# Kernel tuning notes

Hardware: AMD Instinct MI355X
Metric: run time of the kernel (lower is better)

The kernel has to match this reference:

```python
import jax, jax.numpy as jnp
import numpy as np

NUM_DIHEDRALS = 3
# Idealized backbone geometry (picometers / radians), as in RGN/pNeRF.
BOND_LENGTHS = np.array([145.801, 152.326, 132.868], dtype=np.float32)  # N-CA, CA-C, C-N
BOND_ANGLES = np.array([2.124, 1.941, 2.028], dtype=np.float32)


def setup_inputs() -> dict:
    key = jax.random.key(0)
    num_steps, batch = 2048, 512
    flat_dihedrals = jax.random.uniform(
        key, (num_steps * batch, NUM_DIHEDRALS),
        minval=-np.pi, maxval=np.pi, dtype=jnp.float32)
    return {"flat_dihedrals": flat_dihedrals, "batch_size": batch}


def _l2_normalize(v, eps=1e-12):
    return v / jnp.sqrt(jnp.sum(v * v, axis=-1, keepdims=True) + eps)


def dihedral_to_point(dihedral):
    # dihedral: [L, B, 3] -> points in local frames: [3L, B, 3]
    r_cos_theta = np.float32(BOND_LENGTHS * np.cos(np.pi - BOND_ANGLES))  # [3]
    r_sin_theta = np.float32(BOND_LENGTHS * np.sin(np.pi - BOND_ANGLES))  # [3]
    L, B, _ = dihedral.shape
    pt_x = jnp.broadcast_to(jnp.asarray(r_cos_theta), (L, B, NUM_DIHEDRALS))
    pt_y = jnp.cos(dihedral) * r_sin_theta
    pt_z = jnp.sin(dihedral) * r_sin_theta
    point = jnp.stack([pt_x, pt_y, pt_z], axis=-1)      # [L, B, 3, 3]
    return point.reshape(L * NUM_DIHEDRALS, B, 3)       # [3L, B, 3]


def point_to_coordinate(points):
    # points: [N, B, 3]; sequential NeRF rigid-body chain extension.
    B = points.shape[1]
    init = np.array([[-np.sqrt(0.5), np.sqrt(1.5), 0.0],
                     [-np.sqrt(2.0), 0.0, 0.0],
                     [0.0, 0.0, 0.0]], dtype=np.float32)
    a = jnp.broadcast_to(jnp.asarray(init[0]), (B, 3))
    b = jnp.broadcast_to(jnp.asarray(init[1]), (B, 3))
    c = jnp.broadcast_to(jnp.asarray(init[2]), (B, 3))

    def step(carry, p):
        a, b, c = carry
        bc = _l2_normalize(c - b)                      # [B, 3]
        n = _l2_normalize(jnp.cross(b - a, bc))        # [B, 3]
        # Rotation matrix with columns [bc, n x bc, n]
        m = jnp.stack([bc, jnp.cross(n, bc), n], axis=-1)   # [B, 3, 3]
        coord = jnp.einsum('bij,bj->bi', m, p) + c          # [B, 3]
        return (b, c, coord), coord

    _, coords = jax.lax.scan(step, (a, b, c), points)
    return coords  # [N, B, 3]


def reference(flat_dihedrals, batch_size):
    num_steps = flat_dihedrals.shape[0] // batch_size
    dihedrals = flat_dihedrals.reshape(num_steps, batch_size, NUM_DIHEDRALS)
    points = dihedral_to_point(dihedrals)
    coordinates = point_to_coordinate(points)
    return coordinates
```

## Files before the change

kernel.cpp:

```cpp
#include <hip/hip_runtime.h>
#include <math.h>

#define BATCH 512
#define FRAGS 256
#define GROUP 16
#define NGRP  (FRAGS/GROUP)
#define BTILE 32
#define NTILE (BATCH/BTILE)
#define RPF   8
#define READY 0x5EADBEEF

__device__ __forceinline__ void compose(const float* A, const float* B, float* D) {
    float d[12];
    #pragma unroll
    for (int i = 0; i < 3; ++i) {
        #pragma unroll
        for (int j = 0; j < 3; ++j)
            d[i*3+j] = A[i*3+0]*B[0*3+j] + A[i*3+1]*B[1*3+j] + A[i*3+2]*B[2*3+j];
        d[9+i] = A[i*3+0]*B[9] + A[i*3+1]*B[10] + A[i*3+2]*B[11] + A[9+i];
    }
    #pragma unroll
    for (int k = 0; k < 12; ++k) D[k] = d[k];
}

__device__ __forceinline__ void set_identity(float* D) {
    D[0]=1.f; D[1]=0.f; D[2]=0.f;
    D[3]=0.f; D[4]=1.f; D[5]=0.f;
    D[6]=0.f; D[7]=0.f; D[8]=1.f;
    D[9]=0.f; D[10]=0.f; D[11]=0.f;
}

__device__ __forceinline__ void frame_of(
    float ax, float ay, float az,
    float bx, float by, float bz,
    float cx, float cy, float cz,
    float* out )
{
    float bcx = cx - bx, bcy = cy - by, bcz = cz - bz;
    float inv = rsqrtf(bcx*bcx + bcy*bcy + bcz*bcz + 1e-12f);
    bcx *= inv; bcy *= inv; bcz *= inv;
    float bax = bx - ax, bay = by - ay, baz = bz - az;
    float nx = bay*bcz - baz*bcy;
    float ny = baz*bcx - bax*bcz;
    float nz = bax*bcy - bay*bcx;
    inv = rsqrtf(nx*nx + ny*ny + nz*nz + 1e-12f);
    nx *= inv; ny *= inv; nz *= inv;
    float mx = ny*bcz - nz*bcy;
    float my = nz*bcx - nx*bcz;
    float mz = nx*bcy - ny*bcx;
    out[0] = bcx; out[1] = mx; out[2] = nx;
    out[3] = bcy; out[4] = my; out[5] = ny;
    out[6] = bcz; out[7] = mz; out[8] = nz;
    out[9] = cx; out[10] = cy; out[11] = cz;
}

__device__ __forceinline__ void nerf_step(
    float ax, float ay, float az,
    float bx, float by, float bz,
    float cx, float cy, float cz,
    float px, float py, float pz,
    float& ox, float& oy, float& oz)
{
    float bcx = cx - bx, bcy = cy - by, bcz = cz - bz;
    float inv = rsqrtf(bcx*bcx + bcy*bcy + bcz*bcz + 1e-12f);
    bcx *= inv; bcy *= inv; bcz *= inv;
    float bax = bx - ax, bay = by - ay, baz = bz - az;
    float nx = bay*bcz - baz*bcy;
    float ny = baz*bcx - bax*bcz;
    float nz = bax*bcy - bay*bcx;
    inv = rsqrtf(nx*nx + ny*ny + nz*nz + 1e-12f);
    nx *= inv; ny *= inv; nz *= inv;
    float mx = ny*bcz - nz*bcy;
    float my = nz*bcx - nx*bcz;
    float mz = nx*bcy - ny*bcx;
    ox = bcx*px + mx*py + nx*pz + cx;
    oy = bcy*px + my*py + ny*pz + cy;
    oz = bcz*px + mz*py + nz*pz + cz;
}

__device__ __forceinline__ void lane_consts(int b, float* rcl, float* rsl) {
    const float PI = 3.14159265358979323846f;
    float rc[3], rs[3];
    rc[0] = 145.801f * cosf(PI - 2.124f); rs[0] = 145.801f * sinf(PI - 2.124f);
    rc[1] = 152.326f * cosf(PI - 1.941f); rs[1] = 152.326f * sinf(PI - 1.941f);
    rc[2] = 132.868f * cosf(PI - 2.028f); rs[2] = 132.868f * sinf(PI - 2.028f);
    const int d0 = b % 3, d1 = (b + 2) % 3, d2 = (b + 1) % 3;
    rcl[0] = rc[d0]; rcl[1] = rc[d1]; rcl[2] = rc[d2];
    rsl[0] = rs[d0]; rsl[1] = rs[d1]; rsl[2] = rs[d2];
}

__global__ void __launch_bounds__(GROUP * BTILE) coord_onepass(
    const float* __restrict__ dih, float* __restrict__ T,
    int* __restrict__ flags, float* __restrict__ out)
{
    const int btile = blockIdx.x & (NTILE - 1);
    const int g     = blockIdx.x >> 4;
    const int bsub  = threadIdx.x & (BTILE - 1);
    const int j     = threadIdx.x >> 5;
    const int f     = g * GROUP + j;
    const int b     = btile * BTILE + bsub;

    __shared__ float BufA[GROUP * BTILE * 13];
    __shared__ float BufB[GROUP * BTILE * 13];
    float* rowA = &BufA[(size_t)threadIdx.x * 13];
    float* rowB = &BufB[(size_t)threadIdx.x * 13];

    float rcl[3], rsl[3];
    lane_consts(b, rcl, rsl);

    float dd[3 * RPF];
    #pragma unroll
    for (int r = 0; r < RPF; ++r) {
        const float* src = dih + (size_t)(f * RPF + r) * (3 * BATCH) + b;
        dd[r*3 + 0] = __builtin_nontemporal_load(src);
        dd[r*3 + 1] = __builtin_nontemporal_load(src + BATCH);
        dd[r*3 + 2] = __builtin_nontemporal_load(src + 2 * BATCH);
    }

    float lx[3 * RPF], ly[3 * RPF], lz[3 * RPF];

    float ax = -0.70710678118654752f, ay = 1.22474487139158905f, az = 0.0f;
    float bx = -1.41421356237309505f, by = 0.0f, bz = 0.0f;
    float cx = 0.0f, cy = 0.0f, cz = 0.0f;

    #pragma unroll
    for (int r = 0; r < RPF; ++r) {
        #pragma unroll
        for (int k = 0; k < 3; ++k) {
            float sn, cs;
            __sincosf(dd[r*3 + k], &sn, &cs);
            float ox, oy, oz;
            nerf_step(ax, ay, az, bx, by, bz, cx, cy, cz,
                      rcl[k], cs * rsl[k], sn * rsl[k], ox, oy, oz);
            ax = bx; ay = by; az = bz;
            bx = cx; by = cy; bz = cz;
            cx = ox; cy = oy; cz = oz;
            lx[r*3 + k] = ox; ly[r*3 + k] = oy; lz[r*3 + k] = oz;
        }
    }

    float cur[12];
    frame_of(ax, ay, az, bx, by, bz, cx, cy, cz, cur);

    #pragma unroll
    for (int k = 0; k < 12; ++k) rowA[k] = cur[k];
    __syncthreads();
    if (j >= 1) compose(&BufA[(size_t)(threadIdx.x - 1*BTILE) * 13], cur, cur);

    #pragma unroll
    for (int k = 0; k < 12; ++k) rowB[k] = cur[k];
    __syncthreads();
    if (j >= 2) compose(&BufB[(size_t)(threadIdx.x - 2*BTILE) * 13], cur, cur);

    #pragma unroll
    for (int k = 0; k < 12; ++k) rowA[k] = cur[k];
    __syncthreads();
    if (j >= 4) compose(&BufA[(size_t)(threadIdx.x - 4*BTILE) * 13], cur, cur);

    #pragma unroll
    for (int k = 0; k < 12; ++k) rowB[k] = cur[k];
    __syncthreads();
    if (j >= 8) compose(&BufB[(size_t)(threadIdx.x - 8*BTILE) * 13], cur, cur);

    #pragma unroll
    for (int k = 0; k < 12; ++k) rowA[k] = cur[k];
    __syncthreads();

    float pprev[12];
    if (j > 0) {
        #pragma unroll
        for (int k = 0; k < 12; ++k)
            pprev[k] = BufA[(size_t)(threadIdx.x - BTILE) * 13 + k];
    }

    if (j == GROUP - 1 && g < NGRP - 1) {
        #pragma unroll
        for (int k = 0; k < 12; ++k)
            __hip_atomic_store(&T[((size_t)g * 12 + k) * BATCH + b], cur[k],
                               __ATOMIC_RELAXED, __HIP_MEMORY_SCOPE_AGENT);
        if (bsub == 0)
            __hip_atomic_store(&flags[g * NTILE + btile], READY,
                               __ATOMIC_RELEASE, __HIP_MEMORY_SCOPE_AGENT);
    }

    float G[12];
    if (g == 0) {
        if (j == 0) set_identity(G);
        else {
            #pragma unroll
            for (int k = 0; k < 12; ++k) G[k] = pprev[k];
        }
    } else {
        float cur2[12];
        if (j < g) {
            while (__hip_atomic_load(&flags[j * NTILE + btile],
                                     __ATOMIC_ACQUIRE, __HIP_MEMORY_SCOPE_AGENT)
                   != READY) {
                __builtin_amdgcn_s_sleep(1);
            }
            #pragma unroll
            for (int k = 0; k < 12; ++k)
                cur2[k] = __hip_atomic_load(&T[((size_t)j * 12 + k) * BATCH + b],
                                            __ATOMIC_RELAXED, __HIP_MEMORY_SCOPE_AGENT);
        } else {
            set_identity(cur2);
        }

        #pragma unroll
        for (int k = 0; k < 12; ++k) rowB[k] = cur2[k];
        __syncthreads();
        if (j >= 1) compose(&BufB[(size_t)(threadIdx.x - 1*BTILE) * 13], cur2, cur2);

        #pragma unroll
        for (int k = 0; k < 12; ++k) rowA[k] = cur2[k];
        __syncthreads();
        if (j >= 2) compose(&BufA[(size_t)(threadIdx.x - 2*BTILE) * 13], cur2, cur2);

        #pragma unroll
        for (int k = 0; k < 12; ++k) rowB[k] = cur2[k];
        __syncthreads();
        if (j >= 4) compose(&BufB[(size_t)(threadIdx.x - 4*BTILE) * 13], cur2, cur2);

        #pragma unroll
        for (int k = 0; k < 12; ++k) rowA[k] = cur2[k];
        __syncthreads();
        if (j >= 8) compose(&BufA[(size_t)(threadIdx.x - 8*BTILE) * 13], cur2, cur2);

        #pragma unroll
        for (int k = 0; k < 12; ++k) rowB[k] = cur2[k];
        __syncthreads();
        float E[12];
        #pragma unroll
        for (int k = 0; k < 12; ++k)
            E[k] = BufB[(size_t)((g - 1) * BTILE + bsub) * 13 + k];

        if (j == 0) {
            #pragma unroll
            for (int k = 0; k < 12; ++k) G[k] = E[k];
        } else {
            compose(E, pprev, G);
        }
    }

    #pragma unroll
    for (int q = 0; q < 3 * RPF; ++q) {
        float ox = lx[q], oy = ly[q], oz = lz[q];
        float gx = G[0]*ox + G[1]*oy + G[2]*oz + G[9];
        float gy = G[3]*ox + G[4]*oy + G[5]*oz + G[10];
        float gz = G[6]*ox + G[7]*oy + G[8]*oz + G[11];
        size_t n = (size_t)f * (3 * RPF) + q;
        float* dst = out + (n * BATCH + b) * 3;
        __builtin_nontemporal_store(gx, dst + 0);
        __builtin_nontemporal_store(gy, dst + 1);
        __builtin_nontemporal_store(gz, dst + 2);
    }
}

extern "C" void kernel_launch(void* const* d_in, const int* in_sizes, int n_in,
                              void* d_out, int out_size, void* d_ws, size_t ws_size,
                              hipStream_t stream) {
    const float* dih = (const float*)d_in[0];
    float* out = (float*)d_out;
    float* T = (float*)d_ws;
    int* flags = (int*)(T + (size_t)NGRP * 12 * BATCH);

    coord_onepass<<<dim3(NGRP * NTILE), dim3(GROUP * BTILE), 0, stream>>>(
        dih, T, flags, out);
    (void)ws_size; (void)n_in; (void)out_size; (void)in_sizes;
}
```

Baseline: 106.2 us.

## Halve per-fragment work, double group size, and use exclusive scan within groups

Measured after the change: 114.8 us. 1.08x slower.

```diff
diff --git a/kernel.cpp b/kernel.cpp
--- a/kernel.cpp
+++ b/kernel.cpp
@@ -2,12 +2,13 @@
 #include <math.h>
 
 #define BATCH 512
-#define FRAGS 256
-#define GROUP 16
+#define FRAGS 512
+#define GROUP 32
 #define NGRP  (FRAGS/GROUP)
 #define BTILE 32
 #define NTILE (BATCH/BTILE)
-#define RPF   8
+#define RPF   4
+#define NPTS  (3*RPF)
 #define READY 0x5EADBEEF
 
 __device__ __forceinline__ void compose(const float* A, const float* B, float* D) {
@@ -108,16 +109,16 @@
     float rcl[3], rsl[3];
     lane_consts(b, rcl, rsl);
 
-    float dd[3 * RPF];
+    float dd[NPTS];
     #pragma unroll
     for (int r = 0; r < RPF; ++r) {
         const float* src = dih + (size_t)(f * RPF + r) * (3 * BATCH) + b;
-        dd[r*3 + 0] = __builtin_nontemporal_load(src);
-        dd[r*3 + 1] = __builtin_nontemporal_load(src + BATCH);
-        dd[r*3 + 2] = __builtin_nontemporal_load(src + 2 * BATCH);
-    }
-
-    float lx[3 * RPF], ly[3 * RPF], lz[3 * RPF];
+        dd[r*3 + 0] = src[0];
+        dd[r*3 + 1] = src[BATCH];
+        dd[r*3 + 2] = src[2 * BATCH];
+    }
+
+    float lx[NPTS], ly[NPTS], lz[NPTS];
 
     float ax = -0.70710678118654752f, ay = 1.22474487139158905f, az = 0.0f;
     float bx = -1.41421356237309505f, by = 0.0f, bz = 0.0f;
@@ -139,44 +140,51 @@
         }
     }
 
+    float h[12];
+    frame_of(ax, ay, az, bx, by, bz, cx, cy, cz, h);
+
+    #pragma unroll
+    for (int k = 0; k < 12; ++k) rowA[k] = h[k];
+    __syncthreads();
     float cur[12];
-    frame_of(ax, ay, az, bx, by, bz, cx, cy, cz, cur);
+    if (j == 0) set_identity(cur);
+    else {
+        #pragma unroll
+        for (int k = 0; k < 12; ++k)
+            cur[k] = BufA[(size_t)(threadIdx.x - BTILE) * 13 + k];
+    }
+
+    #pragma unroll
+    for (int k = 0; k < 12; ++k) rowB[k] = cur[k];
+    __syncthreads();
+    if (j >= 1) compose(&BufB[(size_t)(threadIdx.x - 1*BTILE) * 13], cur, cur);
 
     #pragma unroll
     for (int k = 0; k < 12; ++k) rowA[k] = cur[k];
     __syncthreads();
-    if (j >= 1) compose(&BufA[(size_t)(threadIdx.x - 1*BTILE) * 13], cur, cur);
+    if (j >= 2) compose(&BufA[(size_t)(threadIdx.x - 2*BTILE) * 13], cur, cur);
 
     #pragma unroll
     for (int k = 0; k < 12; ++k) rowB[k] = cur[k];
     __syncthreads();
-    if (j >= 2) compose(&BufB[(size_t)(threadIdx.x - 2*BTILE) * 13], cur, cur);
+    if (j >= 4) compose(&BufB[(size_t)(threadIdx.x - 4*BTILE) * 13], cur, cur);
 
     #pragma unroll
     for (int k = 0; k < 12; ++k) rowA[k] = cur[k];
     __syncthreads();
-    if (j >= 4) compose(&BufA[(size_t)(threadIdx.x - 4*BTILE) * 13], cur, cur);
+    if (j >= 8) compose(&BufA[(size_t)(threadIdx.x - 8*BTILE) * 13], cur, cur);
 
     #pragma unroll
     for (int k = 0; k < 12; ++k) rowB[k] = cur[k];
     __syncthreads();
-    if (j >= 8) compose(&BufB[(size_t)(threadIdx.x - 8*BTILE) * 13], cur, cur);
-
-    #pragma unroll
-    for (int k = 0; k < 12; ++k) rowA[k] = cur[k];
-    __syncthreads();
-
-    float pprev[12];
-    if (j > 0) {
+    if (j >= 16) compose(&BufB[(size_t)(threadIdx.x - 16*BTILE) * 13], cur, cur);
+
+    if (j == GROUP - 1 && g < NGRP - 1) {
+        float tg[12];
+        compose(cur, h, tg);
         #pragma unroll
         for (int k = 0; k < 12; ++k)
-            pprev[k] = BufA[(size_t)(threadIdx.x - BTILE) * 13 + k];
-    }
-
-    if (j == GROUP - 1 && g < NGRP - 1) {
-        #pragma unroll
-        for (int k = 0; k < 12; ++k)
-            __hip_atomic_store(&T[((size_t)g * 12 + k) * BATCH + b], cur[k],
+            __hip_atomic_store(&T[((size_t)g * 12 + k) * BATCH + b], tg[k],
                                __ATOMIC_RELAXED, __HIP_MEMORY_SCOPE_AGENT);
         if (bsub == 0)
             __hip_atomic_store(&flags[g * NTILE + btile], READY,
@@ -185,11 +193,8 @@
 
     float G[12];
     if (g == 0) {
-        if (j == 0) set_identity(G);
-        else {
-            #pragma unroll
-            for (int k = 0; k < 12; ++k) G[k] = pprev[k];
-        }
+        #pragma unroll
+        for (int k = 0; k < 12; ++k) G[k] = cur[k];
     } else {
         float cur2[12];
         if (j < g) {
@@ -207,52 +212,46 @@
         }
 
         #pragma unroll
+        for (int k = 0; k < 12; ++k) rowA[k] = cur2[k];
+        __syncthreads();
+        if (j >= 1 && j < NGRP) compose(&BufA[(size_t)(threadIdx.x - 1*BTILE) * 13], cur2, cur2);
+
+        #pragma unroll
         for (int k = 0; k < 12; ++k) rowB[k] = cur2[k];
         __syncthreads();
-        if (j >= 1) compose(&BufB[(size_t)(threadIdx.x - 1*BTILE) * 13], cur2, cur2);
+        if (j >= 2 && j < NGRP) compose(&BufB[(size_t)(threadIdx.x - 2*BTILE) * 13], cur2, cur2);
 
         #pragma unroll
         for (int k = 0; k < 12; ++k) rowA[k] = cur2[k];
         __syncthreads();
-        if (j >= 2) compose(&BufA[(size_t)(threadIdx.x - 2*BTILE) * 13], cur2, cur2);
+        if (j >= 4 && j < NGRP) compose(&BufA[(size_t)(threadIdx.x - 4*BTILE) * 13], cur2, cur2);
 
         #pragma unroll
         for (int k = 0; k < 12; ++k) rowB[k] = cur2[k];
         __syncthreads();
-        if (j >= 4) compose(&BufB[(size_t)(threadIdx.x - 4*BTILE) * 13], cur2, cur2);
+        if (j >= 8 && j < NGRP) compose(&BufB[(size_t)(threadIdx.x - 8*BTILE) * 13], cur2, cur2);
 
         #pragma unroll
         for (int k = 0; k < 12; ++k) rowA[k] = cur2[k];
         __syncthreads();
-        if (j >= 8) compose(&BufA[(size_t)(threadIdx.x - 8*BTILE) * 13], cur2, cur2);
-
-        #pragma unroll
-        for (int k = 0; k < 12; ++k) rowB[k] = cur2[k];
-        __syncthreads();
         float E[12];
         #pragma unroll
         for (int k = 0; k < 12; ++k)
-            E[k] = BufB[(size_t)((g - 1) * BTILE + bsub) * 13 + k];
-
-        if (j == 0) {
-            #pragma unroll
-            for (int k = 0; k < 12; ++k) G[k] = E[k];
-        } else {
-            compose(E, pprev, G);
-        }
-    }
-
-    #pragma unroll
-    for (int q = 0; q < 3 * RPF; ++q) {
+            E[k] = BufA[(size_t)((g - 1) * BTILE + bsub) * 13 + k];
+
+        compose(E, cur, G);
+    }
+
+    struct F3 { float x, y, z; };
+    #pragma unroll
+    for (int q = 0; q < NPTS; ++q) {
         float ox = lx[q], oy = ly[q], oz = lz[q];
         float gx = G[0]*ox + G[1]*oy + G[2]*oz + G[9];
         float gy = G[3]*ox + G[4]*oy + G[5]*oz + G[10];
         float gz = G[6]*ox + G[7]*oy + G[8]*oz + G[11];
-        size_t n = (size_t)f * (3 * RPF) + q;
+        size_t n = (size_t)f * NPTS + q;
         float* dst = out + (n * BATCH + b) * 3;
-        __builtin_nontemporal_store(gx, dst + 0);
-        __builtin_nontemporal_store(gy, dst + 1);
-        __builtin_nontemporal_store(gz, dst + 2);
+        *reinterpret_cast<F3*>(dst) = F3{gx, gy, gz};
     }
 }
 
```
